# Optimization experiments

Hardware: AMD Instinct MI355X
Metric: run time of the kernel (lower is better)

Reference implementation:

```python
import jax, jax.numpy as jnp
import numpy as np

DIM = 768
HEADS = 12


def setup_inputs() -> dict:
    key = jax.random.key(0)
    ks = jax.random.split(key, 8)
    B, N, C = 4, 1024, DIM
    x = jax.random.normal(ks[0], (B, N, C), dtype=jnp.float32)
    mask = jax.random.normal(ks[1], (B, 1, N, N), dtype=jnp.float32)
    weight = jax.random.uniform(ks[2], (B, N), dtype=jnp.float32)
    s = 1.0 / np.sqrt(C)
    qkv_w = jax.random.normal(ks[3], (3 * C, C), dtype=jnp.float32) * s
    mu_w = jax.random.normal(ks[4], (C, C // 2), dtype=jnp.float32) * s
    mu_b = jnp.zeros((C,), dtype=jnp.float32)
    ls_w = jax.random.normal(ks[5], (C, C // 2), dtype=jnp.float32) * s
    ls_b = jnp.zeros((C,), dtype=jnp.float32)
    return {"x": x, "mask": mask, "weight": weight, "qkv_w": qkv_w,
            "mu_w": mu_w, "mu_b": mu_b, "ls_w": ls_w, "ls_b": ls_b}


def reference(x, mask, weight, qkv_w, mu_w, mu_b, ls_w, ls_b):
    B, N, C = x.shape
    H = HEADS
    Dh = C // H
    # NOTE: module uses head_dim = dim * num_heads for the scale (quirk, kept faithful)
    scale = (C * H) ** (-0.5)
    qkv = (x @ qkv_w.T).reshape(B, N, 3, H, Dh).transpose(2, 0, 3, 1, 4)  # [3,B,H,N,Dh]
    q, k, v = qkv[0], qkv[1], qkv[2]
    attn = jnp.einsum('bhnd,bhmd->bhnm', q, k) * scale + mask  # [B,H,N,N]
    attn = jax.nn.softmax(attn, axis=-1)
    # weight: [B,N] broadcast over heads and queries (key axis)
    w = weight[:, None, None, :] + 1e-10
    attn = attn * w
    attn = attn / attn.sum(axis=-1, keepdims=True)
    out = jnp.einsum('bhnm,bhmd->bhnd', attn, v)          # [B,H,N,Dh]
    out = out.transpose(0, 2, 1, 3).reshape(B, N, C)      # [B,N,C]
    mu_in = out[:, :, :C // 2]
    ls_in = out[:, :, C // 2:]
    mu = mu_in @ mu_w.T + mu_b
    logsigma = ls_in @ ls_w.T + ls_b
    return (mu, logsigma, attn)
```

## Files before the change

kernel.cpp:

```cpp
#include <hip/hip_runtime.h>
#include <hip/hip_bf16.h>

typedef __attribute__((ext_vector_type(8))) short short8;
typedef __attribute__((ext_vector_type(4))) float f32x4;
typedef __attribute__((ext_vector_type(4))) unsigned short u16x4;

#define NB 4
#define NN 1024
#define NC 768
#define NH 12
#define TC 2304

#define OFF_XB   0ul
#define OFF_WQ   6291456ul
#define OFF_WMU  (OFF_WQ + 3538944ul)
#define OFF_WLS  (OFF_WMU + 589824ul)
#define OFF_QKVB (OFF_WLS + 589824ul)
#define OFF_V3   (OFF_QKVB + 18874368ul)
#define OFF_OUTB (OFF_V3 + 6291456ul)

__device__ __forceinline__ unsigned short f2bf(float f) {
    unsigned int u = __float_as_uint(f);
    u = (u + 0x7FFFu + ((u >> 16) & 1u)) >> 16;
    return (unsigned short)u;
}

__device__ __forceinline__ void gload_lds16(const unsigned short* g, unsigned short* l) {
    __builtin_amdgcn_global_load_lds(
        (const __attribute__((address_space(1))) unsigned int*)g,
        (__attribute__((address_space(3))) unsigned int*)l, 16, 0, 0);
}

__device__ __forceinline__ void gload16(short8& dst, const unsigned short* p) {
    asm volatile("global_load_dwordx4 %0, %1, off" : "=v"(dst) : "v"(p));
}
#define WAITV(N) do { asm volatile("s_waitcnt vmcnt(" #N ")" ::: "memory"); \
                      __builtin_amdgcn_sched_barrier(0); } while (0)
#define SBAR()   __builtin_amdgcn_sched_barrier(0)

__global__ void cast_all(const float* __restrict__ x, const float* __restrict__ qkv_w,
                         const float* __restrict__ mu_w, const float* __restrict__ ls_w,
                         unsigned short* __restrict__ dst) {
    int i = blockIdx.x * blockDim.x + threadIdx.x;
    const float* src; int off;
    if (i < 786432)            { src = x;     off = i; }
    else if (i < 1228800)      { src = qkv_w; off = i - 786432; }
    else if (i < 1302528)      { src = mu_w;  off = i - 1228800; }
    else                       { src = ls_w;  off = i - 1302528; }
    f32x4 v = ((const f32x4*)src)[off];
    u16x4 o;
#pragma unroll
    for (int j = 0; j < 4; ++j) o[j] = f2bf(v[j]);
    ((u16x4*)dst)[i] = o;
}

template <int EPI>
__device__ __forceinline__ void gemm_body(
    unsigned short* As, unsigned short* Bs,
    const unsigned short* __restrict__ A, const unsigned short* __restrict__ Bm,
    int K, int lda, int ldb, void* __restrict__ Cout, int ldc,
    const float* __restrict__ bias, int row0, int col0)
{
    const int t = threadIdx.x;
    const int lane = t & 63;
    const int wv = t >> 6;
    const int wm = wv >> 1, wn = wv & 1;
    const int li = lane & 15;
    const int koff = (lane >> 4) * 8;

    f32x4 acc[4][4] = {};

    const int tr = t >> 2;
    const int tc = (t & 3) * 8;
    const unsigned short* ag = A + (size_t)(row0 + tr) * lda + tc;
    const unsigned short* bg = Bm + (size_t)(col0 + tr) * ldb + tc;

    for (int kt = 0; kt < K; kt += 32) {
        gload_lds16(ag,            As + t * 8);
        gload_lds16(ag + 64 * lda, As + 2048 + t * 8);
        gload_lds16(bg,            Bs + t * 8);
        gload_lds16(bg + 64 * ldb, Bs + 2048 + t * 8);
        ag += 32; bg += 32;
        __syncthreads();
        short8 af[4], bf[4];
#pragma unroll
        for (int m = 0; m < 4; ++m)
            af[m] = *(const short8*)&As[(wm * 64 + m * 16 + li) * 32 + koff];
#pragma unroll
        for (int n = 0; n < 4; ++n)
            bf[n] = *(const short8*)&Bs[(wn * 64 + n * 16 + li) * 32 + koff];
#pragma unroll
        for (int m = 0; m < 4; ++m)
#pragma unroll
            for (int n = 0; n < 4; ++n)
                acc[m][n] = __builtin_amdgcn_mfma_f32_16x16x32_bf16(af[m], bf[n], acc[m][n], 0, 0, 0);
        __syncthreads();
    }

#pragma unroll
    for (int m = 0; m < 4; ++m) {
        const int row = row0 + wm * 64 + m * 16 + (lane >> 4) * 4;
#pragma unroll
        for (int n = 0; n < 4; ++n) {
            const int col = col0 + wn * 64 + n * 16 + li;
#pragma unroll
            for (int r = 0; r < 4; ++r) {
                if (EPI == 0) {
                    ((unsigned short*)Cout)[(size_t)(row + r) * ldc + col] = f2bf(acc[m][n][r]);
                } else {
                    ((float*)Cout)[(size_t)(row + r) * ldc + col] = acc[m][n][r] + bias[col];
                }
            }
        }
    }
}

__global__ __launch_bounds__(256, 2) void gemm_qkv(
    const unsigned short* __restrict__ A, const unsigned short* __restrict__ Bm,
    unsigned short* __restrict__ C)
{
    __shared__ unsigned short As[128 * 32];
    __shared__ unsigned short Bs[128 * 32];
    const int bid = blockIdx.y * gridDim.x + blockIdx.x;
    const int nwg = gridDim.x * gridDim.y;
    const int swz = (bid & 7) * (nwg >> 3) + (bid >> 3);
    const int row0 = (swz / gridDim.x) * 128;
    const int col0 = (swz % gridDim.x) * 128;
    gemm_body<0>(As, Bs, A, Bm, NC, NC, NC, C, TC, nullptr, row0, col0);
}

__global__ __launch_bounds__(256, 2) void gemm_heads(
    const unsigned short* __restrict__ outb,
    const unsigned short* __restrict__ wmu, const unsigned short* __restrict__ wls,
    const float* __restrict__ mu_b, const float* __restrict__ ls_b,
    float* __restrict__ out_mu, float* __restrict__ out_ls)
{
    __shared__ unsigned short As[128 * 32];
    __shared__ unsigned short Bs[128 * 32];
    const int bid = blockIdx.y * gridDim.x + blockIdx.x;
    const int nwg = gridDim.x * gridDim.y;
    const int swz = (bid & 7) * (nwg >> 3) + (bid >> 3);
    const int row0 = (swz / gridDim.x) * 128;
    const int col0 = (swz % gridDim.x) * 128;
    const int z = blockIdx.z;
    gemm_body<1>(As, Bs, outb + (z ? 384 : 0), z ? wls : wmu, 384, NC, 384,
                 z ? (void*)out_ls : (void*)out_mu, NC, z ? ls_b : mu_b, row0, col0);
}

__global__ __launch_bounds__(256, 4) void pack_v(
    const unsigned short* __restrict__ qkvb, unsigned short* __restrict__ v3)
{
    __shared__ unsigned short tile[64][65];
    const int t = threadIdx.x;
    const int bh = blockIdx.y;
    const int b = bh / NH, h = bh % NH;
    const int m0 = blockIdx.x * 64;
#pragma unroll
    for (int i = 0; i < 2; ++i) {
        int lin = i * 256 + t;
        int mr = lin >> 3;
        int dr = (lin & 7) * 8;
        short8 v = *(const short8*)(qkvb + (size_t)(b * NN + m0 + mr) * TC + 1536 + h * 64 + dr);
#pragma unroll
        for (int j = 0; j < 8; ++j) tile[mr][dr + j] = (unsigned short)v[j];
    }
    __syncthreads();
#pragma unroll
    for (int i = 0; i < 2; ++i) {
        int lin = i * 256 + t;
        int dw = lin >> 3;
        int mw = (lin & 7) * 8;
        short8 v;
#pragma unroll
        for (int j = 0; j < 8; ++j) v[j] = (short)tile[mw + j][dw];
        int kt = (m0 + mw) >> 5;
        int mm = mw & 31;
        *(short8*)(v3 + ((size_t)(bh * 32 + kt) * 64 + dw) * 32 + mm) = v;
    }
}

__global__ __launch_bounds__(512, 4) void attn_kernel(
    const unsigned short* __restrict__ qkvb, const unsigned short* __restrict__ v3,
    const float* __restrict__ mask, const float* __restrict__ weight,
    float* __restrict__ attn_out, unsigned short* __restrict__ outb)
{
    __shared__ __align__(16) char smem[66048];
    __shared__ f32x4 po[4][2][64];
    __shared__ float red_max[8][16];
    __shared__ float red_sum[8][16];

    const int t = threadIdx.x;
    const int lane = t & 63;
    const int wv = t >> 6;
    const int li = lane & 15;
    const int g = lane >> 4;
    const int koff = g * 8;
    const int bh = blockIdx.y;
    const int b = bh / NH, h = bh % NH;
    const int n0 = blockIdx.x * 32;
    const int qs = wv >> 2;
    const int ke = wv & 3;

    unsigned short* sm = (unsigned short*)smem;

    const unsigned short* qp = qkvb + (size_t)(b * NN + n0 + qs * 16 + li) * TC + h * 64 + koff;
    short8 qf0 = *(const short8*)qp;
    short8 qf1 = *(const short8*)(qp + 32);

    f32x4 w4 = *(const f32x4*)(weight + b * NN + (lane >> 3) * 128 + ke * 32
                               + ((lane >> 2) & 1) * 16 + (lane & 3) * 4);

    const float* mrow = mask + (size_t)b * NN * NN + (size_t)(n0 + qs * 16 + li) * NN
                      + ke * 32 + g * 4;

    const unsigned short* kgbase = qkvb + (size_t)(b * NN) * TC + 768 + h * 64;

    f32x4 acc[16];
    f32x4 mk[2][2];

    auto stage = [&](int ck) {
#pragma unroll
        for (int i = 0; i < 2; ++i) {
            int m = wv * 16 + i * 8 + (lane >> 3);
            int sl = (lane & 7) ^ (m & 7);
            const unsigned short* src = kgbase + (size_t)(ck * 128 + m) * TC + sl * 8;
            unsigned short* dst = sm + (ck & 1) * 8192 + wv * 1024 + i * 512 + lane * 8;
            gload_lds16(src, dst);
        }
    };

    stage(0);
    mk[0][0] = *(const f32x4*)(mrow);
    mk[0][1] = *(const f32x4*)(mrow + 16);
    __syncthreads();

#pragma unroll
    for (int ck = 0; ck < 8; ++ck) {
        if (ck < 7) {
            stage(ck + 1);
            mk[(ck + 1) & 1][0] = *(const f32x4*)(mrow + (ck + 1) * 128);
            mk[(ck + 1) & 1][1] = *(const f32x4*)(mrow + (ck + 1) * 128 + 16);
        }
        const unsigned short* kbuf = sm + (ck & 1) * 8192;
#pragma unroll
        for (int s = 0; s < 2; ++s) {
            const int m = ke * 32 + s * 16 + li;
            short8 kf0 = *(const short8*)&kbuf[m * 64 + ((g ^ (m & 7)) * 8)];
            short8 kf1 = *(const short8*)&kbuf[m * 64 + (((g + 4) ^ (m & 7)) * 8)];
            f32x4 ci = mk[ck & 1][s] * 96.0f;
            ci = __builtin_amdgcn_mfma_f32_16x16x32_bf16(kf0, qf0, ci, 0, 0, 0);
            ci = __builtin_amdgcn_mfma_f32_16x16x32_bf16(kf1, qf1, ci, 0, 0, 0);
            acc[ck * 2 + s] = ci;
        }
        __syncthreads();
    }

    const float scale = 1.0f / 96.0f;
    float rmax = -1e30f;
#pragma unroll
    for (int cf = 0; cf < 16; ++cf) {
#pragma unroll
        for (int r = 0; r < 4; ++r) rmax = fmaxf(rmax, acc[cf][r]);
    }
    rmax = fmaxf(rmax, __shfl_xor(rmax, 16, 64));
    rmax = fmaxf(rmax, __shfl_xor(rmax, 32, 64));
    if (lane < 16) red_max[wv][lane] = rmax;
    __syncthreads();
    rmax = fmaxf(fmaxf(red_max[qs * 4 + 0][li], red_max[qs * 4 + 1][li]),
                 fmaxf(red_max[qs * 4 + 2][li], red_max[qs * 4 + 3][li])) * scale;

    unsigned short (*P)[1032] = (unsigned short(*)[1032])smem;
    float rsum = 0.f;
#pragma unroll
    for (int cf = 0; cf < 16; ++cf) {
        f32x4 wcf;
#pragma unroll
        for (int r = 0; r < 4; ++r) wcf[r] = __shfl(w4[r], cf * 4 + g, 64);
        u16x4 pb;
#pragma unroll
        for (int r = 0; r < 4; ++r) {
            float p = __expf(acc[cf][r] * scale - rmax) * (wcf[r] + 1e-10f);
            acc[cf][r] = p;
            rsum += p;
            pb[r] = f2bf(p);
        }
        const int col = (cf >> 1) * 128 + ke * 32 + (cf & 1) * 16 + g * 4;
        *(u16x4*)&P[qs * 16 + li][col] = pb;
    }
    rsum += __shfl_xor(rsum, 16, 64);
    rsum += __shfl_xor(rsum, 32, 64);
    if (lane < 16) red_sum[wv][lane] = rsum;
    __syncthreads();

    const int kh = wv >> 2, p4 = wv & 3;
    f32x4 o0 = {}, o1 = {};
    const unsigned short* v3s = v3 + (size_t)bh * 65536 + (size_t)(kh * 16) * 2048
                              + p4 * 512 + li * 32 + g * 8;
    short8 vA[4], vB[4];
#define VISSUE(c, vb2) do {                                                   \
        _Pragma("unroll")                                                     \
        for (int j2 = 0; j2 < 4; ++j2) gload16(vb2[j2], v3s + ((c) * 4 + j2) * 2048); \
    } while (0)
#define VCOMP(c, vb2) do {                                                    \
        _Pragma("unroll")                                                     \
        for (int j2 = 0; j2 < 4; ++j2) {                                      \
            const int kt = kh * 16 + (c) * 4 + j2;                            \
            short8 pa0 = *(const short8*)&P[li][kt * 32 + koff];              \
            short8 pa1 = *(const short8*)&P[16 + li][kt * 32 + koff];         \
            o0 = __builtin_amdgcn_mfma_f32_16x16x32_bf16(pa0, vb2[j2], o0, 0, 0, 0); \
            o1 = __builtin_amdgcn_mfma_f32_16x16x32_bf16(pa1, vb2[j2], o1, 0, 0, 0); \
        }                                                                     \
    } while (0)
    VISSUE(0, vA);
    VISSUE(1, vB);
    WAITV(4);  VCOMP(0, vA); SBAR(); VISSUE(2, vA);
    WAITV(4);  VCOMP(1, vB); SBAR(); VISSUE(3, vB);
    WAITV(4);  VCOMP(2, vA);
    WAITV(0);  VCOMP(3, vB);
#undef VISSUE
#undef VCOMP

    if (kh == 1) { po[p4][0][lane] = o0; po[p4][1][lane] = o1; }
    __syncthreads();
    if (kh == 0) {
        f32x4 q0 = po[p4][0][lane];
        f32x4 q1 = po[p4][1][lane];
        const int dcol = h * 64 + p4 * 16 + li;
#pragma unroll
        for (int r = 0; r < 4; ++r) {
            const int rw = g * 4 + r;
            const float rs0 = red_sum[0][rw] + red_sum[1][rw] + red_sum[2][rw] + red_sum[3][rw];
            const float rs1 = red_sum[4][rw] + red_sum[5][rw] + red_sum[6][rw] + red_sum[7][rw];
            outb[(size_t)(b * NN + n0 + rw) * NC + dcol]      = f2bf((o0[r] + q0[r]) / rs0);
            outb[(size_t)(b * NN + n0 + 16 + rw) * NC + dcol] = f2bf((o1[r] + q1[r]) / rs1);
        }
    }

    const float rinv = 1.0f / (red_sum[qs * 4 + 0][li] + red_sum[qs * 4 + 1][li]
                             + red_sum[qs * 4 + 2][li] + red_sum[qs * 4 + 3][li]);
    float* arow = attn_out + (size_t)bh * NN * NN + (size_t)(n0 + qs * 16 + li) * NN
                + ke * 32 + g * 4;
#pragma unroll
    for (int cf = 0; cf < 16; ++cf) {
        f32x4 a4;
#pragma unroll
        for (int r = 0; r < 4; ++r) a4[r] = acc[cf][r] * rinv;
        __builtin_nontemporal_store(a4, (f32x4*)(arow + (cf >> 1) * 128 + (cf & 1) * 16));
    }
}

extern "C" void kernel_launch(void* const* d_in, const int* in_sizes, int n_in,
                              void* d_out, int out_size, void* d_ws, size_t ws_size,
                              hipStream_t stream) {
    const float* x      = (const float*)d_in[0];
    const float* mask   = (const float*)d_in[1];
    const float* weight = (const float*)d_in[2];
    const float* qkv_w  = (const float*)d_in[3];
    const float* mu_w   = (const float*)d_in[4];
    const float* mu_b   = (const float*)d_in[5];
    const float* ls_w   = (const float*)d_in[6];
    const float* ls_b   = (const float*)d_in[7];

    char* ws = (char*)d_ws;
    unsigned short* xb   = (unsigned short*)(ws + OFF_XB);
    unsigned short* wq   = (unsigned short*)(ws + OFF_WQ);
    unsigned short* wmu  = (unsigned short*)(ws + OFF_WMU);
    unsigned short* wls  = (unsigned short*)(ws + OFF_WLS);
    unsigned short* qkvb = (unsigned short*)(ws + OFF_QKVB);
    unsigned short* v3   = (unsigned short*)(ws + OFF_V3);
    unsigned short* outb = (unsigned short*)(ws + OFF_OUTB);

    float* out_mu   = (float*)d_out;
    float* out_ls   = out_mu + 3145728;
    float* out_attn = out_mu + 6291456;

    cast_all<<<5376, 256, 0, stream>>>(x, qkv_w, mu_w, ls_w, xb);

    gemm_qkv<<<dim3(TC / 128, 4096 / 128), 256, 0, stream>>>(xb, wq, qkvb);

    pack_v<<<dim3(NN / 64, NB * NH), 256, 0, stream>>>(qkvb, v3);

    attn_kernel<<<dim3(NN / 32, NB * NH), 512, 0, stream>>>(
        qkvb, v3, mask, weight, out_attn, outb);

    gemm_heads<<<dim3(NC / 128, 4096 / 128, 2), 256, 0, stream>>>(
        outb, wmu, wls, mu_b, ls_b, out_mu, out_ls);
}
```

Baseline: 151.3 us.

## Double K chunk size, raise MFMA priority, prefetch all V tiles upfront

The QK^T loop now stages 256 keys per step instead of 128, so it runs 4 iterations with 4 barriers instead of 8. Each step loads 4 mask vectors, and the weight, P-column and attn-output indexing is remapped to match. All four V tile groups are issued before any PV compute, which removes the intermediate barriers. s_setprio is raised around the MFMA sections. Launch bounds drop to 2 blocks per SM to leave room for the extra registers, at the risk of less latency hiding from occupancy.

```diff
diff --git a/kernel.cpp b/kernel.cpp
--- a/kernel.cpp
+++ b/kernel.cpp
@@ -179,7 +179,7 @@
     }
 }
 
-__global__ __launch_bounds__(512, 4) void attn_kernel(
+__global__ __launch_bounds__(512, 2) void attn_kernel(
     const unsigned short* __restrict__ qkvb, const unsigned short* __restrict__ v3,
     const float* __restrict__ mask, const float* __restrict__ weight,
     float* __restrict__ attn_out, unsigned short* __restrict__ outb)
@@ -207,51 +207,52 @@
     short8 qf0 = *(const short8*)qp;
     short8 qf1 = *(const short8*)(qp + 32);
 
-    f32x4 w4 = *(const f32x4*)(weight + b * NN + (lane >> 3) * 128 + ke * 32
-                               + ((lane >> 2) & 1) * 16 + (lane & 3) * 4);
+    f32x4 w4 = *(const f32x4*)(weight + b * NN + (lane >> 4) * 256 + ke * 64 + (lane & 15) * 4);
 
     const float* mrow = mask + (size_t)b * NN * NN + (size_t)(n0 + qs * 16 + li) * NN
-                      + ke * 32 + g * 4;
+                      + ke * 64 + g * 4;
 
     const unsigned short* kgbase = qkvb + (size_t)(b * NN) * TC + 768 + h * 64;
 
     f32x4 acc[16];
-    f32x4 mk[2][2];
+    f32x4 mk[2][4];
 
     auto stage = [&](int ck) {
 #pragma unroll
-        for (int i = 0; i < 2; ++i) {
-            int m = wv * 16 + i * 8 + (lane >> 3);
+        for (int i = 0; i < 4; ++i) {
+            int m = wv * 32 + i * 8 + (lane >> 3);
             int sl = (lane & 7) ^ (m & 7);
-            const unsigned short* src = kgbase + (size_t)(ck * 128 + m) * TC + sl * 8;
-            unsigned short* dst = sm + (ck & 1) * 8192 + wv * 1024 + i * 512 + lane * 8;
+            const unsigned short* src = kgbase + (size_t)(ck * 256 + m) * TC + sl * 8;
+            unsigned short* dst = sm + (ck & 1) * 16384 + wv * 2048 + i * 512 + lane * 8;
             gload_lds16(src, dst);
         }
     };
+    auto mload = [&](int ck) {
+#pragma unroll
+        for (int s = 0; s < 4; ++s)
+            mk[ck & 1][s] = *(const f32x4*)(mrow + ck * 256 + s * 16);
+    };
 
     stage(0);
-    mk[0][0] = *(const f32x4*)(mrow);
-    mk[0][1] = *(const f32x4*)(mrow + 16);
-    __syncthreads();
-
-#pragma unroll
-    for (int ck = 0; ck < 8; ++ck) {
-        if (ck < 7) {
-            stage(ck + 1);
-            mk[(ck + 1) & 1][0] = *(const f32x4*)(mrow + (ck + 1) * 128);
-            mk[(ck + 1) & 1][1] = *(const f32x4*)(mrow + (ck + 1) * 128 + 16);
-        }
-        const unsigned short* kbuf = sm + (ck & 1) * 8192;
-#pragma unroll
-        for (int s = 0; s < 2; ++s) {
-            const int m = ke * 32 + s * 16 + li;
+    mload(0);
+    __syncthreads();
+
+#pragma unroll
+    for (int ck = 0; ck < 4; ++ck) {
+        if (ck < 3) { stage(ck + 1); mload(ck + 1); }
+        const unsigned short* kbuf = sm + (ck & 1) * 16384;
+        __builtin_amdgcn_s_setprio(1);
+#pragma unroll
+        for (int s = 0; s < 4; ++s) {
+            const int m = ke * 64 + s * 16 + li;
             short8 kf0 = *(const short8*)&kbuf[m * 64 + ((g ^ (m & 7)) * 8)];
             short8 kf1 = *(const short8*)&kbuf[m * 64 + (((g + 4) ^ (m & 7)) * 8)];
             f32x4 ci = mk[ck & 1][s] * 96.0f;
             ci = __builtin_amdgcn_mfma_f32_16x16x32_bf16(kf0, qf0, ci, 0, 0, 0);
             ci = __builtin_amdgcn_mfma_f32_16x16x32_bf16(kf1, qf1, ci, 0, 0, 0);
-            acc[ck * 2 + s] = ci;
-        }
+            acc[ck * 4 + s] = ci;
+        }
+        __builtin_amdgcn_s_setprio(0);
         __syncthreads();
     }
 
@@ -284,7 +285,7 @@
             rsum += p;
             pb[r] = f2bf(p);
         }
-        const int col = (cf >> 1) * 128 + ke * 32 + (cf & 1) * 16 + g * 4;
+        const int col = (cf >> 2) * 256 + ke * 64 + (cf & 3) * 16 + g * 4;
         *(u16x4*)&P[qs * 16 + li][col] = pb;
     }
     rsum += __shfl_xor(rsum, 16, 64);
@@ -296,12 +297,13 @@
     f32x4 o0 = {}, o1 = {};
     const unsigned short* v3s = v3 + (size_t)bh * 65536 + (size_t)(kh * 16) * 2048
                               + p4 * 512 + li * 32 + g * 8;
-    short8 vA[4], vB[4];
+    short8 vA[4], vB[4], vC[4], vD[4];
 #define VISSUE(c, vb2) do {                                                   \
         _Pragma("unroll")                                                     \
         for (int j2 = 0; j2 < 4; ++j2) gload16(vb2[j2], v3s + ((c) * 4 + j2) * 2048); \
     } while (0)
 #define VCOMP(c, vb2) do {                                                    \
+        __builtin_amdgcn_s_setprio(1);                                        \
         _Pragma("unroll")                                                     \
         for (int j2 = 0; j2 < 4; ++j2) {                                      \
             const int kt = kh * 16 + (c) * 4 + j2;                            \
@@ -310,13 +312,13 @@
             o0 = __builtin_amdgcn_mfma_f32_16x16x32_bf16(pa0, vb2[j2], o0, 0, 0, 0); \
             o1 = __builtin_amdgcn_mfma_f32_16x16x32_bf16(pa1, vb2[j2], o1, 0, 0, 0); \
         }                                                                     \
+        __builtin_amdgcn_s_setprio(0);                                        \
     } while (0)
-    VISSUE(0, vA);
-    VISSUE(1, vB);
-    WAITV(4);  VCOMP(0, vA); SBAR(); VISSUE(2, vA);
-    WAITV(4);  VCOMP(1, vB); SBAR(); VISSUE(3, vB);
-    WAITV(4);  VCOMP(2, vA);
-    WAITV(0);  VCOMP(3, vB);
+    VISSUE(0, vA); VISSUE(1, vB); VISSUE(2, vC); VISSUE(3, vD);
+    WAITV(12); VCOMP(0, vA);
+    WAITV(8);  VCOMP(1, vB);
+    WAITV(4);  VCOMP(2, vC);
+    WAITV(0);  VCOMP(3, vD);
 #undef VISSUE
 #undef VCOMP
 
@@ -339,13 +341,13 @@
     const float rinv = 1.0f / (red_sum[qs * 4 + 0][li] + red_sum[qs * 4 + 1][li]
                              + red_sum[qs * 4 + 2][li] + red_sum[qs * 4 + 3][li]);
     float* arow = attn_out + (size_t)bh * NN * NN + (size_t)(n0 + qs * 16 + li) * NN
-                + ke * 32 + g * 4;
+                + ke * 64 + g * 4;
 #pragma unroll
     for (int cf = 0; cf < 16; ++cf) {
         f32x4 a4;
 #pragma unroll
         for (int r = 0; r < 4; ++r) a4[r] = acc[cf][r] * rinv;
-        __builtin_nontemporal_store(a4, (f32x4*)(arow + (cf >> 1) * 128 + (cf & 1) * 16));
+        __builtin_nontemporal_store(a4, (f32x4*)(arow + (cf >> 2) * 256 + (cf & 3) * 16));
     }
 }
 
```

New measurement: 163.0 us. 7.7% more time.

## Halve attention query tile to 16 rows for higher occupancy

Applied to the files above, without the earlier changes.

The attention kernel now handles 16 query rows per block instead of 32. Each of its 8 waves covers a 16-key slice of every 128-key chunk, which halves the accumulator registers and shared memory and raises the launch bound to 6 blocks per CU. The attn output store moves ahead of the PV matmul, weights are loaded directly instead of shuffled, and setprio wraps the PV MFMAs. In exchange K and V are loaded twice as often across blocks, and each wave does fewer MFMAs per K tile.

```diff
diff --git a/kernel.cpp b/kernel.cpp
--- a/kernel.cpp
+++ b/kernel.cpp
@@ -179,13 +179,13 @@
     }
 }
 
-__global__ __launch_bounds__(512, 4) void attn_kernel(
+__global__ __launch_bounds__(512, 6) void attn_kernel(
     const unsigned short* __restrict__ qkvb, const unsigned short* __restrict__ v3,
     const float* __restrict__ mask, const float* __restrict__ weight,
     float* __restrict__ attn_out, unsigned short* __restrict__ outb)
 {
-    __shared__ __align__(16) char smem[66048];
-    __shared__ f32x4 po[4][2][64];
+    __shared__ __align__(16) char smem[33024];
+    __shared__ f32x4 po[4][64];
     __shared__ float red_max[8][16];
     __shared__ float red_sum[8][16];
 
@@ -197,26 +197,19 @@
     const int koff = g * 8;
     const int bh = blockIdx.y;
     const int b = bh / NH, h = bh % NH;
-    const int n0 = blockIdx.x * 32;
-    const int qs = wv >> 2;
-    const int ke = wv & 3;
+    const int n0 = blockIdx.x * 16;
 
     unsigned short* sm = (unsigned short*)smem;
 
-    const unsigned short* qp = qkvb + (size_t)(b * NN + n0 + qs * 16 + li) * TC + h * 64 + koff;
+    const unsigned short* qp = qkvb + (size_t)(b * NN + n0 + li) * TC + h * 64 + koff;
     short8 qf0 = *(const short8*)qp;
     short8 qf1 = *(const short8*)(qp + 32);
 
-    f32x4 w4 = *(const f32x4*)(weight + b * NN + (lane >> 3) * 128 + ke * 32
-                               + ((lane >> 2) & 1) * 16 + (lane & 3) * 4);
-
-    const float* mrow = mask + (size_t)b * NN * NN + (size_t)(n0 + qs * 16 + li) * NN
-                      + ke * 32 + g * 4;
-
+    const float* mrow = mask + (size_t)b * NN * NN + (size_t)(n0 + li) * NN + wv * 16 + g * 4;
     const unsigned short* kgbase = qkvb + (size_t)(b * NN) * TC + 768 + h * 64;
 
-    f32x4 acc[16];
-    f32x4 mk[2][2];
+    f32x4 acc[8];
+    f32x4 mk[2];
 
     auto stage = [&](int ck) {
 #pragma unroll
@@ -230,35 +223,29 @@
     };
 
     stage(0);
-    mk[0][0] = *(const f32x4*)(mrow);
-    mk[0][1] = *(const f32x4*)(mrow + 16);
+    mk[0] = *(const f32x4*)(mrow);
     __syncthreads();
 
 #pragma unroll
     for (int ck = 0; ck < 8; ++ck) {
         if (ck < 7) {
             stage(ck + 1);
-            mk[(ck + 1) & 1][0] = *(const f32x4*)(mrow + (ck + 1) * 128);
-            mk[(ck + 1) & 1][1] = *(const f32x4*)(mrow + (ck + 1) * 128 + 16);
+            mk[(ck + 1) & 1] = *(const f32x4*)(mrow + (ck + 1) * 128);
         }
         const unsigned short* kbuf = sm + (ck & 1) * 8192;
-#pragma unroll
-        for (int s = 0; s < 2; ++s) {
-            const int m = ke * 32 + s * 16 + li;
-            short8 kf0 = *(const short8*)&kbuf[m * 64 + ((g ^ (m & 7)) * 8)];
-            short8 kf1 = *(const short8*)&kbuf[m * 64 + (((g + 4) ^ (m & 7)) * 8)];
-            f32x4 ci = mk[ck & 1][s] * 96.0f;
-            ci = __builtin_amdgcn_mfma_f32_16x16x32_bf16(kf0, qf0, ci, 0, 0, 0);
-            ci = __builtin_amdgcn_mfma_f32_16x16x32_bf16(kf1, qf1, ci, 0, 0, 0);
-            acc[ck * 2 + s] = ci;
-        }
+        short8 kf0 = *(const short8*)&kbuf[(wv * 16 + li) * 64 + ((g ^ (li & 7)) * 8)];
+        short8 kf1 = *(const short8*)&kbuf[(wv * 16 + li) * 64 + (((g + 4) ^ (li & 7)) * 8)];
+        f32x4 ci = mk[ck & 1] * 96.0f;
+        ci = __builtin_amdgcn_mfma_f32_16x16x32_bf16(kf0, qf0, ci, 0, 0, 0);
+        ci = __builtin_amdgcn_mfma_f32_16x16x32_bf16(kf1, qf1, ci, 0, 0, 0);
+        acc[ck] = ci;
         __syncthreads();
     }
 
     const float scale = 1.0f / 96.0f;
     float rmax = -1e30f;
 #pragma unroll
-    for (int cf = 0; cf < 16; ++cf) {
+    for (int cf = 0; cf < 8; ++cf) {
 #pragma unroll
         for (int r = 0; r < 4; ++r) rmax = fmaxf(rmax, acc[cf][r]);
     }
@@ -266,16 +253,20 @@
     rmax = fmaxf(rmax, __shfl_xor(rmax, 32, 64));
     if (lane < 16) red_max[wv][lane] = rmax;
     __syncthreads();
-    rmax = fmaxf(fmaxf(red_max[qs * 4 + 0][li], red_max[qs * 4 + 1][li]),
-                 fmaxf(red_max[qs * 4 + 2][li], red_max[qs * 4 + 3][li])) * scale;
+    {
+        float m01 = fmaxf(red_max[0][li], red_max[1][li]);
+        float m23 = fmaxf(red_max[2][li], red_max[3][li]);
+        float m45 = fmaxf(red_max[4][li], red_max[5][li]);
+        float m67 = fmaxf(red_max[6][li], red_max[7][li]);
+        rmax = fmaxf(fmaxf(m01, m23), fmaxf(m45, m67)) * scale;
+    }
 
     unsigned short (*P)[1032] = (unsigned short(*)[1032])smem;
+    const float* wbase = weight + b * NN + wv * 16 + g * 4;
     float rsum = 0.f;
 #pragma unroll
-    for (int cf = 0; cf < 16; ++cf) {
-        f32x4 wcf;
-#pragma unroll
-        for (int r = 0; r < 4; ++r) wcf[r] = __shfl(w4[r], cf * 4 + g, 64);
+    for (int cf = 0; cf < 8; ++cf) {
+        f32x4 wcf = *(const f32x4*)(wbase + cf * 128);
         u16x4 pb;
 #pragma unroll
         for (int r = 0; r < 4; ++r) {
@@ -284,16 +275,27 @@
             rsum += p;
             pb[r] = f2bf(p);
         }
-        const int col = (cf >> 1) * 128 + ke * 32 + (cf & 1) * 16 + g * 4;
-        *(u16x4*)&P[qs * 16 + li][col] = pb;
+        *(u16x4*)&P[li][cf * 128 + wv * 16 + g * 4] = pb;
     }
     rsum += __shfl_xor(rsum, 16, 64);
     rsum += __shfl_xor(rsum, 32, 64);
     if (lane < 16) red_sum[wv][lane] = rsum;
     __syncthreads();
 
+    const float rinv = 1.0f / (red_sum[0][li] + red_sum[1][li] + red_sum[2][li]
+                             + red_sum[3][li] + red_sum[4][li] + red_sum[5][li]
+                             + red_sum[6][li] + red_sum[7][li]);
+    float* arow = attn_out + (size_t)bh * NN * NN + (size_t)(n0 + li) * NN + wv * 16 + g * 4;
+#pragma unroll
+    for (int cf = 0; cf < 8; ++cf) {
+        f32x4 a4;
+#pragma unroll
+        for (int r = 0; r < 4; ++r) a4[r] = acc[cf][r] * rinv;
+        __builtin_nontemporal_store(a4, (f32x4*)(arow + cf * 128));
+    }
+
     const int kh = wv >> 2, p4 = wv & 3;
-    f32x4 o0 = {}, o1 = {};
+    f32x4 o = {};
     const unsigned short* v3s = v3 + (size_t)bh * 65536 + (size_t)(kh * 16) * 2048
                               + p4 * 512 + li * 32 + g * 8;
     short8 vA[4], vB[4];
@@ -302,14 +304,14 @@
         for (int j2 = 0; j2 < 4; ++j2) gload16(vb2[j2], v3s + ((c) * 4 + j2) * 2048); \
     } while (0)
 #define VCOMP(c, vb2) do {                                                    \
+        __builtin_amdgcn_s_setprio(1);                                        \
         _Pragma("unroll")                                                     \
         for (int j2 = 0; j2 < 4; ++j2) {                                      \
             const int kt = kh * 16 + (c) * 4 + j2;                            \
-            short8 pa0 = *(const short8*)&P[li][kt * 32 + koff];              \
-            short8 pa1 = *(const short8*)&P[16 + li][kt * 32 + koff];         \
-            o0 = __builtin_amdgcn_mfma_f32_16x16x32_bf16(pa0, vb2[j2], o0, 0, 0, 0); \
-            o1 = __builtin_amdgcn_mfma_f32_16x16x32_bf16(pa1, vb2[j2], o1, 0, 0, 0); \
+            short8 pa = *(const short8*)&P[li][kt * 32 + koff];               \
+            o = __builtin_amdgcn_mfma_f32_16x16x32_bf16(pa, vb2[j2], o, 0, 0, 0); \
         }                                                                     \
+        __builtin_amdgcn_s_setprio(0);                                        \
     } while (0)
     VISSUE(0, vA);
     VISSUE(1, vB);
@@ -320,32 +322,19 @@
 #undef VISSUE
 #undef VCOMP
 
-    if (kh == 1) { po[p4][0][lane] = o0; po[p4][1][lane] = o1; }
+    if (kh == 1) po[p4][lane] = o;
     __syncthreads();
     if (kh == 0) {
-        f32x4 q0 = po[p4][0][lane];
-        f32x4 q1 = po[p4][1][lane];
+        f32x4 oo = po[p4][lane];
         const int dcol = h * 64 + p4 * 16 + li;
 #pragma unroll
         for (int r = 0; r < 4; ++r) {
-            const int rw = g * 4 + r;
-            const float rs0 = red_sum[0][rw] + red_sum[1][rw] + red_sum[2][rw] + red_sum[3][rw];
-            const float rs1 = red_sum[4][rw] + red_sum[5][rw] + red_sum[6][rw] + red_sum[7][rw];
-            outb[(size_t)(b * NN + n0 + rw) * NC + dcol]      = f2bf((o0[r] + q0[r]) / rs0);
-            outb[(size_t)(b * NN + n0 + 16 + rw) * NC + dcol] = f2bf((o1[r] + q1[r]) / rs1);
-        }
-    }
-
-    const float rinv = 1.0f / (red_sum[qs * 4 + 0][li] + red_sum[qs * 4 + 1][li]
-                             + red_sum[qs * 4 + 2][li] + red_sum[qs * 4 + 3][li]);
-    float* arow = attn_out + (size_t)bh * NN * NN + (size_t)(n0 + qs * 16 + li) * NN
-                + ke * 32 + g * 4;
-#pragma unroll
-    for (int cf = 0; cf < 16; ++cf) {
-        f32x4 a4;
-#pragma unroll
-        for (int r = 0; r < 4; ++r) a4[r] = acc[cf][r] * rinv;
-        __builtin_nontemporal_store(a4, (f32x4*)(arow + (cf >> 1) * 128 + (cf & 1) * 16));
+            const int row = g * 4 + r;
+            const float rs = red_sum[0][row] + red_sum[1][row] + red_sum[2][row]
+                           + red_sum[3][row] + red_sum[4][row] + red_sum[5][row]
+                           + red_sum[6][row] + red_sum[7][row];
+            outb[(size_t)(b * NN + n0 + row) * NC + dcol] = f2bf((o[r] + oo[r]) / rs);
+        }
     }
 }
 
@@ -380,7 +369,7 @@
 
     pack_v<<<dim3(NN / 64, NB * NH), 256, 0, stream>>>(qkvb, v3);
 
-    attn_kernel<<<dim3(NN / 32, NB * NH), 512, 0, stream>>>(
+    attn_kernel<<<dim3(NN / 16, NB * NH), 512, 0, stream>>>(
         qkvb, v3, mask, weight, out_attn, outb);
 
     gemm_heads<<<dim3(NC / 128, 4096 / 128, 2), 256, 0, stream>>>(
```

New measurement: 144.7 us. 1.05x faster.
